# Performance work log

Hardware: AMD Instinct MI355X
Metric: run time of the kernel (lower is better)

Reference implementation:

```python
import jax, jax.numpy as jnp
import numpy as np

K = 4
TEMPERATURE = 30.0


def setup_inputs() -> dict:
    key = jax.random.key(0)
    ks = jax.random.split(key, 6)
    B, C, H, W_sp = 32, 128, 56, 56
    Cout, kh, kw = 128, 3, 3
    Cred = max(C // 4, 1)
    x = jax.random.normal(ks[0], (B, C, H, W_sp), dtype=jnp.float32)
    # K parallel conv kernels + biases (fan-in scaled init)
    fan = C * kh * kw
    W = jax.random.normal(ks[1], (K, Cout, C, kh, kw), dtype=jnp.float32) / np.sqrt(fan)
    b = jax.random.normal(ks[2], (K, Cout), dtype=jnp.float32) * 0.01
    # attention branch: 1x1 convs == dense on pooled features
    aw1 = jax.random.normal(ks[3], (Cred, C), dtype=jnp.float32) / np.sqrt(C)
    aw2 = jax.random.normal(ks[4], (K, Cred), dtype=jnp.float32) / np.sqrt(Cred)
    return {"x": x, "W": W, "b": b, "aw1": aw1, "aw2": aw2}


def reference(x, W, b, aw1, aw2):
    # attention: global avg pool -> 1x1 conv (dense) -> relu -> 1x1 conv -> softmax(logits/T)
    pooled = jnp.mean(x, axis=(2, 3))                       # [B, C]
    h1 = jax.nn.relu(jnp.einsum('bc,rc->br', pooled, aw1))  # [B, Cred]
    logits = jnp.einsum('br,kr->bk', h1, aw2)               # [B, K]
    attn = jax.nn.softmax(logits / TEMPERATURE, axis=1)     # [B, K]

    pad = 1
    out = None
    for i in range(K):  # fixed small K, structurally distinct kernels
        yi = jax.lax.conv_general_dilated(
            x, W[i], window_strides=(1, 1), padding=[(pad, pad), (pad, pad)],
            dimension_numbers=('NCHW', 'OIHW', 'NCHW'))
        yi = yi + b[i][None, :, None, None]
        yi = yi * attn[:, i][:, None, None, None]
        out = yi if out is None else out + yi
    return out
```

## Files before the change

kernel.cpp:

```cpp
#include <hip/hip_runtime.h>
#include <hip/hip_bf16.h>
#include <stdint.h>

typedef __bf16 bf16x8 __attribute__((ext_vector_type(8)));
typedef float  f32x4  __attribute__((ext_vector_type(4)));
typedef unsigned short u16x8 __attribute__((ext_vector_type(8)));
typedef unsigned int   u32x4 __attribute__((ext_vector_type(4)));

#define NB 32
#define NC 128
#define NH 56
#define NW 56
#define NK 4
#define NCO 128
#define NCR 32
#define NHW 3136
#define TEMPER 30.0f

#define WS_ATTN   0u
#define WS_BC     4096u
#define WS_ROWSUM 65536u
#define WS_WC     1048576u
#define WS_XT     10485760u

__global__ void xt_kernel(const float* __restrict__ x, __hip_bfloat16* __restrict__ xt,
                          float* __restrict__ rowsum) {
  __shared__ float lds[58 * 133];
  int xcd = blockIdx.x & 7;
  int j   = blockIdx.x >> 3;
  int b   = xcd * 4 + j / 58;
  int hp  = j % 58;
  int blk = b * 58 + hp;
  int h = hp - 1;
  bool hin = (h >= 0) && (h < NH);
  int tid = threadIdx.x;
  if (hin) {
    const float* xrow = x + ((size_t)b * NC) * NHW + (size_t)h * NW;
    for (int i = tid; i < 128 * 14; i += 256) {
      int c = i / 14;
      int w4 = (i - c * 14) * 4;
      float4 v = *(const float4*)(xrow + (size_t)c * NHW + w4);
      int base = (w4 + 1) * 133 + c;
      lds[base]         = v.x;
      lds[base + 133]   = v.y;
      lds[base + 2*133] = v.z;
      lds[base + 3*133] = v.w;
    }
  }
  __syncthreads();
  __hip_bfloat16* orow = xt + (size_t)blk * (58 * 128);
  for (int i = tid; i < 58 * 16; i += 256) {
    int wp = i >> 4;
    int cg = (i & 15) << 3;
    u16x8 o;
    if (!hin || wp == 0 || wp == 57) {
      o = (u16x8)0;
    } else {
      const float* src = lds + wp * 133 + cg;
      #pragma unroll
      for (int jx = 0; jx < 8; ++jx) {
        union { __hip_bfloat16 b; unsigned short u; } cv;
        cv.b = __float2bfloat16(src[jx]);
        o[jx] = cv.u;
      }
    }
    *(u16x8*)(orow + wp * 128 + cg) = o;
  }
  if (hin && tid < 128) {
    float s = 0.f;
    #pragma unroll 8
    for (int wp = 1; wp <= 56; ++wp) s += lds[wp * 133 + tid];
    rowsum[(size_t)blk * 128 + tid] = s;
  }
}

__global__ void attn_kernel(const float* __restrict__ rowsum, const float* __restrict__ aw1,
                            const float* __restrict__ aw2, const float* __restrict__ bias,
                            float* __restrict__ attn, float* __restrict__ bc_out) {
  int b = blockIdx.x;
  __shared__ float sp[NC], h1[NCR], at[NK];
  int t = threadIdx.x;
  if (t < NC) {
    float s = 0.f;
    for (int hp = 1; hp <= 56; ++hp) s += rowsum[((size_t)b * 58 + hp) * 128 + t];
    sp[t] = s * (1.0f / (float)NHW);
  }
  __syncthreads();
  if (t < NCR) {
    float s = 0.f;
    for (int c = 0; c < NC; ++c) s += aw1[t*NC + c] * sp[c];
    h1[t] = s > 0.f ? s : 0.f;
  }
  __syncthreads();
  if (t == 0) {
    float lg[NK], mx = -1e30f;
    for (int k = 0; k < NK; ++k) {
      float s = 0.f;
      for (int r = 0; r < NCR; ++r) s += aw2[k*NCR + r] * h1[r];
      lg[k] = s * (1.0f/TEMPER);
      mx = fmaxf(mx, lg[k]);
    }
    float den = 0.f, e[NK];
    for (int k = 0; k < NK; ++k) { e[k] = expf(lg[k]-mx); den += e[k]; }
    float inv = 1.0f/den;
    for (int k = 0; k < NK; ++k) { at[k] = e[k]*inv; attn[b*NK+k] = at[k]; }
  }
  __syncthreads();
  if (t < NCO) {
    float s = 0.f;
    for (int k = 0; k < NK; ++k) s += at[k] * bias[k*NCO + t];
    bc_out[b*NCO + t] = s;
  }
}

__global__ void combine_kernel(const float* __restrict__ W, const float* __restrict__ attn,
                               __hip_bfloat16* __restrict__ wc) {
  int gid = blockIdx.x;
  int bg  = gid >> 6;
  int tcell = (gid & 63) * 256 + threadIdx.x;
  int co = tcell >> 7, ci = tcell & 127;
  float w[4][9];
  const float* wp = W + ((size_t)co * 128 + ci) * 9;
  #pragma unroll
  for (int k = 0; k < 4; ++k)
    #pragma unroll
    for (int j = 0; j < 9; ++j)
      w[k][j] = wp[(size_t)k * 147456 + j];
  for (int b = bg * 8; b < bg * 8 + 8; ++b) {
    float a0 = attn[b*4+0], a1 = attn[b*4+1], a2 = attn[b*4+2], a3 = attn[b*4+3];
    #pragma unroll
    for (int j = 0; j < 9; ++j) {
      float v = a0*w[0][j] + a1*w[1][j] + a2*w[2][j] + a3*w[3][j];
      wc[(((size_t)b*9 + j) * 128 + co) * 128 + ci] = __float2bfloat16(v);
    }
  }
}

#define RS 2368
#define CS 40
#define ACS 40
#define AKWS (128*ACS)

#define GLOAD16(src, dst) \
  __builtin_amdgcn_global_load_lds( \
    (const __attribute__((address_space(1))) unsigned int*)(src), \
    (__attribute__((address_space(3))) unsigned int*)(dst), 16, 0, 0)

__global__ __launch_bounds__(256, 2) void conv_kernel(
    const unsigned short* __restrict__ xt,
    const unsigned short* __restrict__ wc,
    const float* __restrict__ bc,
    float* __restrict__ out) {
  __shared__ __align__(16) unsigned short lds_b[1792*8];
  __shared__ __align__(16) unsigned short lds_a[3*AKWS];
  const int tid  = threadIdx.x;
  const int lane = tid & 63;
  const int wv   = tid >> 6;
  const int wm   = wv & 1;
  const int wn   = wv >> 1;
  const int bid  = blockIdx.x;
  const int xcd  = bid & 7;
  const int jj   = bid >> 3;
  const int b    = xcd*4 + jj/14;
  const int r0   = (jj % 14) * 4;
  const int li   = lane & 15;
  const int kg   = lane >> 4;

  int srcB[7];
  #pragma unroll
  for (int i = 0; i < 7; ++i) {
    int q = i*256 + tid;
    int r = q / 296;
    int sl = q - r*296;
    int col = sl / 5;
    int part = sl - col*5;
    int rc = r > 5 ? 5 : r;
    int cl = col > 57 ? 57 : col;
    int pc = part > 3 ? 3 : part;
    srcB[i] = ((r0 + rc)*58 + cl)*128 + pc*8;
  }
  int srcA[6], dstA[6];
  #pragma unroll
  for (int i = 0; i < 6; ++i) {
    int c = i*256 + tid;
    int kwl  = c >> 9;
    int co   = (c & 511) >> 2;
    int part = c & 3;
    srcA[i] = (kwl*128 + co)*128 + part*8;
    dstA[i] = kwl*AKWS + co*ACS + part*8;
  }

  int xoff[7];
  #pragma unroll
  for (int f = 0; f < 7; ++f) {
    int pos = wn*112 + f*16 + li;
    int rB = pos / 56;
    int cB = pos - rB*56;
    xoff[f] = rB*RS + cB*CS + kg*8;
  }
  const int aRead = (wm*64 + li)*ACS + kg*8;

  const f32x4 vzero = {0.f, 0.f, 0.f, 0.f};
  f32x4 acc[4][7];
  #pragma unroll
  for (int mo = 0; mo < 4; ++mo)
    #pragma unroll
    for (int f = 0; f < 7; ++f) acc[mo][f] = vzero;

  const unsigned short* xtg = xt + (size_t)b*(58*58*128);
  const unsigned short* wcg = wc + (size_t)b*(9*128*128);

  for (int cc = 0; cc < 4; ++cc) {
    #pragma unroll
    for (int kh = 0; kh < 3; ++kh) {
      u32x4 areg[6];
      #pragma unroll
      for (int i = 0; i < 6; ++i)
        areg[i] = *(const u32x4*)(wcg + kh*49152 + srcA[i] + cc*32);
      __syncthreads();
      if (kh == 0) {
        #pragma unroll
        for (int i = 0; i < 7; ++i)
          GLOAD16(xtg + srcB[i] + cc*32, lds_b + (i*256 + wv*64)*8);
      }
      #pragma unroll
      for (int i = 0; i < 6; ++i)
        *(u32x4*)(lds_a + dstA[i]) = areg[i];
      __syncthreads();
      #pragma unroll
      for (int kwl = 0; kwl < 3; ++kwl) {
        bf16x8 af[4];
        #pragma unroll
        for (int mo = 0; mo < 4; ++mo)
          af[mo] = *(const bf16x8*)(lds_a + kwl*AKWS + aRead + mo*(16*ACS));
        bf16x8 bfr[7];
        #pragma unroll
        for (int f = 0; f < 7; ++f)
          bfr[f] = *(const bf16x8*)(lds_b + xoff[f] + kh*RS + kwl*CS);
        #pragma unroll
        for (int mo = 0; mo < 4; ++mo)
          #pragma unroll
          for (int f = 0; f < 7; ++f)
            acc[mo][f] = __builtin_amdgcn_mfma_f32_16x16x32_bf16(af[mo], bfr[f], acc[mo][f], 0, 0, 0);
      }
    }
  }

  float* ob = out + (size_t)b*NCO*NHW;
  #pragma unroll
  for (int mo = 0; mo < 4; ++mo) {
    #pragma unroll
    for (int rg = 0; rg < 4; ++rg) {
      const int co = wm*64 + mo*16 + kg*4 + rg;
      const float bv = bc[b*NCO + co];
      float* orow = ob + (size_t)co*NHW;
      #pragma unroll
      for (int f = 0; f < 7; ++f) {
        int pos = wn*112 + f*16 + li;
        int rB = pos / 56;
        int cB = pos - rB*56;
        orow[(r0 + rB)*56 + cB] = acc[mo][f][rg] + bv;
      }
    }
  }
}

extern "C" void kernel_launch(void* const* d_in, const int* in_sizes, int n_in,
                              void* d_out, int out_size, void* d_ws, size_t ws_size,
                              hipStream_t stream) {
  const float* x   = (const float*)d_in[0];
  const float* W   = (const float*)d_in[1];
  const float* bia = (const float*)d_in[2];
  const float* aw1 = (const float*)d_in[3];
  const float* aw2 = (const float*)d_in[4];
  float* out = (float*)d_out;
  char* ws = (char*)d_ws;
  float* attn   = (float*)(ws + WS_ATTN);
  float* bcm    = (float*)(ws + WS_BC);
  float* rowsum = (float*)(ws + WS_ROWSUM);
  __hip_bfloat16* wc = (__hip_bfloat16*)(ws + WS_WC);
  __hip_bfloat16* xt = (__hip_bfloat16*)(ws + WS_XT);

  xt_kernel<<<NB*58, 256, 0, stream>>>(x, xt, rowsum);
  attn_kernel<<<NB, 128, 0, stream>>>(rowsum, aw1, aw2, bia, attn, bcm);
  combine_kernel<<<256, 256, 0, stream>>>(W, attn, wc);
  conv_kernel<<<448, 256, 0, stream>>>((const unsigned short*)xt,
                                       (const unsigned short*)wc, bcm, out);
}
```

Before: 66.26 us.

## Load weights directly to LDS and double-buffer fragments with MFMA priority

Replaces the register-staged weight copy (global load to registers, then LDS store with padded stride) with direct global_load_lds into an unpadded LDS layout. The inner kwl loop is restructured into a ping-pong of register fragments so LDS reads for the next kwl overlap MFMA work on the current one. Wave priority is raised around the MFMA groups and extra s_barrier calls are inserted to keep waves in step. The unpadded A layout (stride 32) can cause LDS bank conflicts on fragment reads, and the extra barriers may add stalls.

```diff
diff --git a/kernel.cpp b/kernel.cpp
--- a/kernel.cpp
+++ b/kernel.cpp
@@ -5,7 +5,6 @@
 typedef __bf16 bf16x8 __attribute__((ext_vector_type(8)));
 typedef float  f32x4  __attribute__((ext_vector_type(4)));
 typedef unsigned short u16x8 __attribute__((ext_vector_type(8)));
-typedef unsigned int   u32x4 __attribute__((ext_vector_type(4)));
 
 #define NB 32
 #define NC 128
@@ -138,8 +137,6 @@
 
 #define RS 2368
 #define CS 40
-#define ACS 40
-#define AKWS (128*ACS)
 
 #define GLOAD16(src, dst) \
   __builtin_amdgcn_global_load_lds( \
@@ -152,7 +149,7 @@
     const float* __restrict__ bc,
     float* __restrict__ out) {
   __shared__ __align__(16) unsigned short lds_b[1792*8];
-  __shared__ __align__(16) unsigned short lds_a[3*AKWS];
+  __shared__ __align__(16) unsigned short lds_a[3*4096];
   const int tid  = threadIdx.x;
   const int lane = tid & 63;
   const int wv   = tid >> 6;
@@ -179,7 +176,7 @@
     int pc = part > 3 ? 3 : part;
     srcB[i] = ((r0 + rc)*58 + cl)*128 + pc*8;
   }
-  int srcA[6], dstA[6];
+  int srcA[6];
   #pragma unroll
   for (int i = 0; i < 6; ++i) {
     int c = i*256 + tid;
@@ -187,7 +184,6 @@
     int co   = (c & 511) >> 2;
     int part = c & 3;
     srcA[i] = (kwl*128 + co)*128 + part*8;
-    dstA[i] = kwl*AKWS + co*ACS + part*8;
   }
 
   int xoff[7];
@@ -198,7 +194,7 @@
     int cB = pos - rB*56;
     xoff[f] = rB*RS + cB*CS + kg*8;
   }
-  const int aRead = (wm*64 + li)*ACS + kg*8;
+  const int aRead = (wm*64 + li)*32 + kg*8;
 
   const f32x4 vzero = {0.f, 0.f, 0.f, 0.f};
   f32x4 acc[4][7];
@@ -210,39 +206,49 @@
   const unsigned short* xtg = xt + (size_t)b*(58*58*128);
   const unsigned short* wcg = wc + (size_t)b*(9*128*128);
 
+  #define LOADFRAG(AF, BF, kwl, kh) do { \
+    _Pragma("unroll") \
+    for (int mo = 0; mo < 4; ++mo) \
+      AF[mo] = *(const bf16x8*)(lds_a + (kwl)*4096 + aRead + mo*512); \
+    _Pragma("unroll") \
+    for (int f = 0; f < 7; ++f) \
+      BF[f] = *(const bf16x8*)(lds_b + xoff[f] + (kh)*RS + (kwl)*CS); \
+  } while (0)
+
+  #define PRIO_MFMA(AF, BF) do { \
+    __builtin_amdgcn_s_setprio(1); \
+    _Pragma("unroll") \
+    for (int mo = 0; mo < 4; ++mo) \
+      _Pragma("unroll") \
+      for (int f = 0; f < 7; ++f) \
+        acc[mo][f] = __builtin_amdgcn_mfma_f32_16x16x32_bf16(AF[mo], BF[f], acc[mo][f], 0, 0, 0); \
+    __builtin_amdgcn_s_setprio(0); \
+  } while (0)
+
   for (int cc = 0; cc < 4; ++cc) {
     #pragma unroll
     for (int kh = 0; kh < 3; ++kh) {
-      u32x4 areg[6];
+      __syncthreads();
       #pragma unroll
       for (int i = 0; i < 6; ++i)
-        areg[i] = *(const u32x4*)(wcg + kh*49152 + srcA[i] + cc*32);
-      __syncthreads();
+        GLOAD16(wcg + kh*49152 + srcA[i] + cc*32, lds_a + (i*256 + wv*64)*8);
       if (kh == 0) {
         #pragma unroll
         for (int i = 0; i < 7; ++i)
           GLOAD16(xtg + srcB[i] + cc*32, lds_b + (i*256 + wv*64)*8);
       }
-      #pragma unroll
-      for (int i = 0; i < 6; ++i)
-        *(u32x4*)(lds_a + dstA[i]) = areg[i];
       __syncthreads();
-      #pragma unroll
-      for (int kwl = 0; kwl < 3; ++kwl) {
-        bf16x8 af[4];
-        #pragma unroll
-        for (int mo = 0; mo < 4; ++mo)
-          af[mo] = *(const bf16x8*)(lds_a + kwl*AKWS + aRead + mo*(16*ACS));
-        bf16x8 bfr[7];
-        #pragma unroll
-        for (int f = 0; f < 7; ++f)
-          bfr[f] = *(const bf16x8*)(lds_b + xoff[f] + kh*RS + kwl*CS);
-        #pragma unroll
-        for (int mo = 0; mo < 4; ++mo)
-          #pragma unroll
-          for (int f = 0; f < 7; ++f)
-            acc[mo][f] = __builtin_amdgcn_mfma_f32_16x16x32_bf16(af[mo], bfr[f], acc[mo][f], 0, 0, 0);
-      }
+
+      bf16x8 afE[4], bfE[7], afO[4], bfO[7];
+      LOADFRAG(afE, bfE, 0, kh);
+      __builtin_amdgcn_s_barrier();
+      LOADFRAG(afO, bfO, 1, kh);
+      PRIO_MFMA(afE, bfE);
+      __builtin_amdgcn_s_barrier();
+      LOADFRAG(afE, bfE, 2, kh);
+      PRIO_MFMA(afO, bfO);
+      __builtin_amdgcn_s_barrier();
+      PRIO_MFMA(afE, bfE);
     }
   }
 
```

Result: no change. 66.80 us, median of 2 (+0.8%).
